# Performance work log

Measured on AMD Instinct MI355X. Metric: run time of the kernel, lower is better.

## Reference

```python
import jax, jax.numpy as jnp
import numpy as np

N, E, G = 20000, 640000, 64
D_IN, H, C, D_OUT = 256, 4, 64, 32
HC = H * C


def gat_layer(x, W, a_src, a_dst, b, src, dst, n_nodes, heads, ch):
    # x: [N, F_in], W: [F_in, H*C]
    h = (x @ W).reshape(n_nodes, heads, ch)          # [N,H,C]
    es = jnp.einsum('nhc,hc->nh', h, a_src)          # [N,H]
    ed = jnp.einsum('nhc,hc->nh', h, a_dst)
    e = jax.nn.leaky_relu(es[src] + ed[dst], 0.2)    # [Etot,H]
    m = jax.ops.segment_max(e, dst, num_segments=n_nodes)
    m = jnp.where(jnp.isfinite(m), m, 0.0)
    ex = jnp.exp(e - m[dst])
    denom = jax.ops.segment_sum(ex, dst, num_segments=n_nodes)
    alpha = ex / jnp.maximum(denom[dst], 1e-16)      # softmax over in-edges per dst
    out = jax.ops.segment_sum(alpha[:, :, None] * h[src], dst, num_segments=n_nodes)
    return out.reshape(n_nodes, heads * ch) + b


def setup_inputs() -> dict:
    key = jax.random.key(0)
    ks = jax.random.split(key, 14)
    g1 = 1.0 / np.sqrt(D_IN)
    g2 = 1.0 / np.sqrt(HC)
    inp = {
        'x': jax.random.normal(ks[0], (N, D_IN), jnp.float32),
        'edge_index': jax.random.randint(ks[1], (2, E), 0, N, jnp.int64 if jax.config.jax_enable_x64 else jnp.int32),
        'batch': jnp.sort(jax.random.randint(ks[2], (N,), 0, G)),
        'W1': jax.random.normal(ks[3], (D_IN, HC), jnp.float32) * g1,
        'a_src1': jax.random.normal(ks[4], (H, C), jnp.float32) * g2,
        'a_dst1': jax.random.normal(ks[5], (H, C), jnp.float32) * g2,
        'b1': jnp.zeros((HC,), jnp.float32),
        'W2': jax.random.normal(ks[6], (HC, HC), jnp.float32) * g2,
        'a_src2': jax.random.normal(ks[7], (H, C), jnp.float32) * g2,
        'a_dst2': jax.random.normal(ks[8], (H, C), jnp.float32) * g2,
        'b2': jnp.zeros((HC,), jnp.float32),
        'Wp': jax.random.normal(ks[9], (HC, D_OUT), jnp.float32) * g2,
        'bp': jnp.zeros((D_OUT,), jnp.float32),
    }
    return inp


def reference(x, edge_index, batch, W1, a_src1, a_dst1, b1, W2, a_src2, a_dst2, b2, Wp, bp):
    # add self-loops (PyG GATConv default)
    loop = jnp.arange(N, dtype=edge_index.dtype)
    src = jnp.concatenate([edge_index[0], loop])
    dst = jnp.concatenate([edge_index[1], loop])
    x1 = jax.nn.relu(gat_layer(x, W1, a_src1, a_dst1, b1, src, dst, N, H, C))
    # dropout p=0.6 is identity in eval mode
    x2 = jax.nn.relu(gat_layer(x1, W2, a_src2, a_dst2, b2, src, dst, N, H, C))
    node_scores = x2 @ Wp + bp                        # [N, D_OUT]
    sums = jax.ops.segment_sum(node_scores, batch, num_segments=G)
    counts = jax.ops.segment_sum(jnp.ones((N,), node_scores.dtype), batch, num_segments=G)
    return sums / jnp.maximum(counts, 1.0)[:, None]   # [G, D_OUT]
```

## Files before the change

### kernel.cpp

```cpp
#include <hip/hip_runtime.h>
#include <hip/hip_bf16.h>
#include <cstdint>

#define NNODES 20000
#define NEDGES 640000
#define ETOT   (NEDGES + NNODES)
#define NGROUP 64
#define HC     256
#define DOUT   32
#define EBLK   5120
#define NBLK   (NEDGES / EBLK)
#define CBLK   ((NNODES + 255) / 256)
#define GBLK   (NNODES / 16)
#define GPITCH 1280

typedef short bf16x8 __attribute__((ext_vector_type(8)));
typedef short s16x4  __attribute__((ext_vector_type(4)));
typedef float f32x4  __attribute__((ext_vector_type(4)));
typedef float f32x2  __attribute__((ext_vector_type(2)));
typedef int   s32x4  __attribute__((ext_vector_type(4)));
typedef unsigned int u32x4 __attribute__((ext_vector_type(4)));

__device__ __forceinline__ float b2f(__hip_bfloat16 v) { return __bfloat162float(v); }
__device__ __forceinline__ float bs2f(short v) {
    union { unsigned int u; float f; } c; c.u = ((unsigned int)(unsigned short)v) << 16; return c.f;
}
__device__ __forceinline__ short f2bs(float v) {
    __hip_bfloat16 b = __float2bfloat16(v);
    union { __hip_bfloat16 b; short s; } u; u.b = b; return u.s;
}
__device__ __forceinline__ float ldf(const void* __restrict__ p, size_t i, int bf) {
    return bf ? __bfloat162float(((const __hip_bfloat16*)p)[i]) : ((const float*)p)[i];
}
__device__ __forceinline__ int ld_idx(const int* __restrict__ p, size_t i, int f64) {
    return f64 ? p[2 * i] : p[i];
}
__device__ __forceinline__ int probe_edge64(const int* __restrict__ ei) {
    int l = threadIdx.x & 63;
    int zeros = 0;
#pragma unroll
    for (int r = 0; r < 4; r++)
        zeros += __popcll(__ballot(ei[2 * (r * 64 + l) + 1] == 0));
    return (zeros > 200) ? 1 : 0;
}
__device__ __forceinline__ int probe_xbf(const unsigned int* __restrict__ xw) {
    int l = threadIdx.x & 63;
    int ones = 0;
#pragma unroll
    for (int r = 0; r < 4; r++)
        ones += __popcll(__ballot((xw[r * 64 + l] >> 14) & 1));
    return (ones < 64) ? 1 : 0;
}

__global__ __launch_bounds__(256) void k_setup(const unsigned int* __restrict__ xw,
                                               const int* __restrict__ ei,
                                               const void* __restrict__ W1, const void* __restrict__ W2,
                                               __hip_bfloat16* __restrict__ Wt1,
                                               __hip_bfloat16* __restrict__ Wt2,
                                               int* __restrict__ H,
                                               float* __restrict__ sx, int* __restrict__ cnt,
                                               int* __restrict__ flag) {
    __shared__ int hl[NNODES];
    int t = threadIdx.x, b = blockIdx.x;
    if (b < NBLK) {
        int f = probe_edge64(ei);
        s32x4* hl4 = reinterpret_cast<s32x4*>(hl);
        for (int i = t; i < NNODES / 4; i += 256) hl4[i] = (s32x4){0, 0, 0, 0};
        __syncthreads();
        int s0 = b * EBLK;
        if (f) {
            const int* d64 = ei + 2 * NEDGES;
            for (int i0 = s0; i0 < s0 + EBLK; i0 += 512) {
                int i = i0 + 2 * t;
                s32x4 v = *reinterpret_cast<const s32x4*>(d64 + 2 * (size_t)i);
                atomicAdd(&hl[v[0]], 1);
                atomicAdd(&hl[v[2]], 1);
            }
        } else {
            const int* d32 = ei + NEDGES;
            for (int i0 = s0; i0 < s0 + EBLK; i0 += 1024) {
                int i = i0 + 4 * t;
                s32x4 v = *reinterpret_cast<const s32x4*>(d32 + i);
                atomicAdd(&hl[v[0]], 1); atomicAdd(&hl[v[1]], 1);
                atomicAdd(&hl[v[2]], 1); atomicAdd(&hl[v[3]], 1);
            }
        }
        __syncthreads();
        s32x4* Hb4 = reinterpret_cast<s32x4*>(H + (size_t)b * NNODES);
        for (int i = t; i < NNODES / 4; i += 256) Hb4[i] = hl4[i];
    } else {
        int bf = probe_xbf(xw);
        int i = (b - NBLK) * 256 + t;
        int which = i >> 16;
        int j = i & 65535;
        int k = j >> 8, n = j & 255;
        const void* W = which ? W2 : W1;
        __hip_bfloat16* Wt = which ? Wt2 : Wt1;
        Wt[(size_t)n * 256 + k] = __float2bfloat16(ldf(W, (size_t)k * 256 + n, bf));
        if (b == NBLK) {
            for (int q = t; q < NGROUP * HC; q += 256) sx[q] = 0.f;
            if (t < NGROUP) cnt[t] = 0;
            int f = probe_edge64(ei);
            if (t == 0) { flag[0] = f; flag[1] = bf; }
        }
    }
}

__global__ __launch_bounds__(256) void k_colsum(const int* __restrict__ H,
                                                int* __restrict__ deg,
                                                int* __restrict__ bsum) {
    __shared__ int wred[4];
    int t = threadIdx.x, n = blockIdx.x * 256 + t;
    int s = 0;
    if (n < NNODES) {
#pragma unroll 5
        for (int b = 0; b < NBLK; b++) s += H[(size_t)b * NNODES + n];
        s += 1;
        deg[n] = s;
    }
    int r = s;
#pragma unroll
    for (int o = 1; o < 64; o <<= 1) r += __shfl_xor(r, o);
    if ((t & 63) == 0) wred[t >> 6] = r;
    __syncthreads();
    if (t == 0) bsum[blockIdx.x] = wred[0] + wred[1] + wred[2] + wred[3];
}

__global__ __launch_bounds__(256) void k_base(int* __restrict__ H,
                                              const int* __restrict__ deg,
                                              const int* __restrict__ bsum,
                                              int* __restrict__ off,
                                              int* __restrict__ csr) {
    __shared__ int wtot[4];
    __shared__ int boff_s;
    int t = threadIdx.x, blk = blockIdx.x;
    int n = blk * 256 + t;
    int d = (n < NNODES) ? deg[n] : 0;
    int lane = t & 63, w = t >> 6;
    int sc = d;
#pragma unroll
    for (int o = 1; o < 64; o <<= 1) {
        int u = __shfl_up(sc, o);
        if (lane >= o) sc += u;
    }
    if (lane == 63) wtot[w] = sc;
    if (w == 0) {
        int v = (lane < blk) ? bsum[lane] : 0;
        if (lane + 64 < blk) v += bsum[lane + 64];
#pragma unroll
        for (int o = 1; o < 64; o <<= 1) v += __shfl_xor(v, o);
        if (lane == 0) boff_s = v;
    }
    __syncthreads();
    int woff = 0;
    for (int i = 0; i < w; i++) woff += wtot[i];
    int excl = woff + sc - d;
    if (blk == 0 && t == 0) off[NNODES] = ETOT;
    if (n < NNODES) {
        int o0 = boff_s + excl;
        off[n] = o0;
        csr[o0] = n;
        int run = o0 + 1;
#pragma unroll 5
        for (int b = 0; b < NBLK; b++) {
            size_t idx = (size_t)b * NNODES + n;
            int tt = H[idx];
            H[idx] = run;
            run += tt;
        }
    }
}

__global__ __launch_bounds__(256) void k_scatter2(const int* __restrict__ ei,
                                                  const int* __restrict__ H,
                                                  int* __restrict__ csr,
                                                  const int* __restrict__ flag) {
    __shared__ int base_l[NNODES];
    int t = threadIdx.x, b = blockIdx.x, f = flag[0];
    const s32x4* Hb4 = reinterpret_cast<const s32x4*>(H + (size_t)b * NNODES);
    s32x4* bl4 = reinterpret_cast<s32x4*>(base_l);
    for (int i = t; i < NNODES / 4; i += 256) bl4[i] = Hb4[i];
    __syncthreads();
    int s0 = b * EBLK;
    if (f) {
        const int* d64 = ei + 2 * NEDGES;
        for (int i0 = s0; i0 < s0 + EBLK; i0 += 512) {
            int i = i0 + 2 * t;
            s32x4 sv = *reinterpret_cast<const s32x4*>(ei + 2 * (size_t)i);
            s32x4 dv = *reinterpret_cast<const s32x4*>(d64 + 2 * (size_t)i);
            int p0 = atomicAdd(&base_l[dv[0]], 1);
            csr[p0] = sv[0];
            int p1 = atomicAdd(&base_l[dv[2]], 1);
            csr[p1] = sv[2];
        }
    } else {
        const int* d32 = ei + NEDGES;
        for (int i0 = s0; i0 < s0 + EBLK; i0 += 1024) {
            int i = i0 + 4 * t;
            s32x4 sv = *reinterpret_cast<const s32x4*>(ei + i);
            s32x4 dv = *reinterpret_cast<const s32x4*>(d32 + i);
#pragma unroll
            for (int k = 0; k < 4; k++) {
                int p = atomicAdd(&base_l[dv[k]], 1);
                csr[p] = sv[k];
            }
        }
    }
}

__global__ __launch_bounds__(256) void k_gemm(const void* __restrict__ A,
                                              const __hip_bfloat16* __restrict__ Bt,
                                              __hip_bfloat16* __restrict__ Hout,
                                              const void* __restrict__ a_src,
                                              const void* __restrict__ a_dst,
                                              float* __restrict__ es4, float* __restrict__ ed4,
                                              float* __restrict__ gpart,
                                              const int* __restrict__ flag, int force_bf) {
    __shared__ u32x4 hst4[512];
    int bf   = flag[1];
    int abf  = force_bf | bf;
    int w    = threadIdx.x >> 6;
    int lane = threadIdx.x & 63;
    int mr   = lane & 15;
    int quad = lane >> 4;
    int r0   = blockIdx.x * 16;
    f32x4 acc[4];
#pragma unroll
    for (int j = 0; j < 4; j++) acc[j] = (f32x4){0.f, 0.f, 0.f, 0.f};
    size_t rowoff = (size_t)(r0 + mr) * HC;
    const __hip_bfloat16* Btw = Bt + (size_t)w * 64 * HC;
    for (int kk = 0; kk < HC; kk += 32) {
        bf16x8 a;
        if (abf) {
            a = *reinterpret_cast<const bf16x8*>((const __hip_bfloat16*)A + rowoff + kk + quad * 8);
        } else {
            const float* af = (const float*)A + rowoff + kk + quad * 8;
            f32x4 lo = *reinterpret_cast<const f32x4*>(af);
            f32x4 hi = *reinterpret_cast<const f32x4*>(af + 4);
#pragma unroll
            for (int ii = 0; ii < 4; ii++) { a[ii] = f2bs(lo[ii]); a[ii + 4] = f2bs(hi[ii]); }
        }
#pragma unroll
        for (int j = 0; j < 4; j++) {
            bf16x8 b = *reinterpret_cast<const bf16x8*>(Btw + (size_t)(j * 16 + mr) * HC + kk + quad * 8);
            acc[j] = __builtin_amdgcn_mfma_f32_16x16x32_bf16(a, b, acc[j], 0, 0, 0);
        }
    }
    short* hst = reinterpret_cast<short*>(hst4);
#pragma unroll
    for (int j = 0; j < 4; j++)
#pragma unroll
        for (int r = 0; r < 4; r++)
            hst[(quad * 4 + r) * HC + w * 64 + j * 16 + mr] = f2bs(acc[j][r]);
    float ps[4] = {0.f, 0.f, 0.f, 0.f}, pd[4] = {0.f, 0.f, 0.f, 0.f};
#pragma unroll
    for (int j = 0; j < 4; j++) {
        float asv = ldf(a_src, (size_t)(w * 64 + j * 16 + mr), bf);
        float adv = ldf(a_dst, (size_t)(w * 64 + j * 16 + mr), bf);
#pragma unroll
        for (int r = 0; r < 4; r++) {
            ps[r] = fmaf(acc[j][r], asv, ps[r]);
            pd[r] = fmaf(acc[j][r], adv, pd[r]);
        }
    }
#pragma unroll
    for (int o = 1; o < 16; o <<= 1)
#pragma unroll
        for (int r = 0; r < 4; r++) {
            ps[r] += __shfl_xor(ps[r], o);
            pd[r] += __shfl_xor(pd[r], o);
        }
    float pm = fmaxf(fmaxf(ps[0], ps[1]), fmaxf(ps[2], ps[3]));
    pm = fmaxf(pm, __shfl_xor(pm, 16));
    pm = fmaxf(pm, __shfl_xor(pm, 32));
    if (lane == 0) gpart[w * GPITCH + blockIdx.x] = pm;
    if (mr == 0)
#pragma unroll
        for (int r = 0; r < 4; r++) {
            int row = r0 + quad * 4 + r;
            es4[(size_t)row * 4 + w] = ps[r];
            ed4[(size_t)row * 4 + w] = pd[r];
        }
    __syncthreads();
    u32x4* dst = reinterpret_cast<u32x4*>((short*)Hout + (size_t)r0 * HC);
    dst[threadIdx.x]       = hst4[threadIdx.x];
    dst[threadIdx.x + 256] = hst4[threadIdx.x + 256];
}

__global__ __launch_bounds__(256) void k_agg(const __hip_bfloat16* __restrict__ Hb,
                                             const float* __restrict__ es4, const float* __restrict__ ed4,
                                             const void* __restrict__ bias,
                                             const int* __restrict__ off, const int* __restrict__ csr,
                                             const float* __restrict__ gpart,
                                             const int* __restrict__ flag,
                                             __hip_bfloat16* __restrict__ out) {
    __shared__ float p_lds[4][4][64];
    __shared__ int   s_lds[4][64];
    __shared__ float gm_lds[4];
    int wv = threadIdx.x >> 6;
    int l  = threadIdx.x & 63;
    int half = l >> 5;
    int hl   = l & 31;
    int hd8  = hl >> 3;
    int bf = flag[1];
    {
        float m = -INFINITY;
        for (int i = l; i < GBLK; i += 64) m = fmaxf(m, gpart[wv * GPITCH + i]);
#pragma unroll
        for (int o = 32; o; o >>= 1) m = fmaxf(m, __shfl_xor(m, o));
        if (l == 0) gm_lds[wv] = m;
    }
    __syncthreads();
    f32x4 gm = (f32x4){gm_lds[0], gm_lds[1], gm_lds[2], gm_lds[3]};
    int n0 = blockIdx.x * 4 + wv;
    for (int n = n0; n < NNODES; n += 10000) {
        int base = off[n], deg = off[n + 1] - base;
        f32x4 edv = *reinterpret_cast<const f32x4*>(ed4 + (size_t)n * 4);
        f32x4 M;
#pragma unroll
        for (int h = 0; h < 4; h++) {
            float t0 = gm[h] + edv[h];
            M[h] = (t0 > 0.f) ? t0 : 0.2f * t0;
        }
        f32x4 dsum = (f32x4){0.f, 0.f, 0.f, 0.f};
        f32x2 acc2[4];
#pragma unroll
        for (int d = 0; d < 4; d++) acc2[d] = (f32x2){0.f, 0.f};
        for (int c0 = 0; c0 < deg; c0 += 64) {
            int cn = min(deg - c0, 64);
            int s = 0;
            f32x4 pv = (f32x4){0.f, 0.f, 0.f, 0.f};
            if (l < cn) {
                s = csr[base + c0 + l];
                f32x4 e = *reinterpret_cast<const f32x4*>(es4 + (size_t)s * 4);
#pragma unroll
                for (int h = 0; h < 4; h++) {
                    float t = e[h] + edv[h];
                    t = (t > 0.f) ? t : 0.2f * t;
                    pv[h] = __expf(t - M[h]);
                }
            }
            s_lds[wv][l] = s;
#pragma unroll
            for (int h = 0; h < 4; h++) p_lds[wv][h][l] = pv[h];
#pragma unroll
            for (int h = 0; h < 4; h++) dsum[h] += pv[h];
            int jn = (cn + 15) & ~15;
            for (int j = 0; j < jn; j += 16) {
                int e0 = j + 8 * half;
                s32x4 sA = *reinterpret_cast<const s32x4*>(&s_lds[wv][e0]);
                s32x4 sB = *reinterpret_cast<const s32x4*>(&s_lds[wv][e0 + 4]);
                f32x4 pA = *reinterpret_cast<const f32x4*>(&p_lds[wv][hd8][e0]);
                f32x4 pB = *reinterpret_cast<const f32x4*>(&p_lds[wv][hd8][e0 + 4]);
                u32x4 hv[8];
#pragma unroll
                for (int i = 0; i < 8; i++) {
                    int sj = (i < 4) ? sA[i & 3] : sB[i & 3];
                    hv[i] = *reinterpret_cast<const u32x4*>(Hb + (size_t)sj * HC + hl * 8);
                }
#pragma unroll
                for (int i = 0; i < 8; i++) {
                    float p = (i < 4) ? pA[i & 3] : pB[i & 3];
#pragma unroll
                    for (int d = 0; d < 4; d++) {
                        unsigned int u = hv[i][d];
                        f32x2 h2;
                        h2.x = __uint_as_float(u << 16);
                        h2.y = __uint_as_float(u & 0xFFFF0000u);
                        acc2[d] += h2 * p;
                    }
                }
            }
        }
#pragma unroll
        for (int o = 32; o; o >>= 1)
#pragma unroll
            for (int h = 0; h < 4; h++) dsum[h] += __shfl_xor(dsum[h], o);
#pragma unroll
        for (int d = 0; d < 4; d++) {
            acc2[d].x += __shfl_xor(acc2[d].x, 32);
            acc2[d].y += __shfl_xor(acc2[d].y, 32);
        }
        float rinv = 1.0f / fmaxf(dsum[hd8], 1e-16f);
        if (half == 0) {
            bf16x8 ov;
#pragma unroll
            for (int d = 0; d < 4; d++) {
                float v0 = acc2[d].x * rinv + ldf(bias, (size_t)hl * 8 + 2 * d, bf);
                float v1 = acc2[d].y * rinv + ldf(bias, (size_t)hl * 8 + 2 * d + 1, bf);
                ov[2 * d]     = f2bs(fmaxf(v0, 0.f));
                ov[2 * d + 1] = f2bs(fmaxf(v1, 0.f));
            }
            *reinterpret_cast<bf16x8*>(out + (size_t)n * HC + hl * 8) = ov;
        }
    }
}

__global__ __launch_bounds__(256) void k_groupsum(const __hip_bfloat16* __restrict__ X2,
                                                  const int* __restrict__ batch,
                                                  float* __restrict__ sx, int* __restrict__ cnt,
                                                  const int* __restrict__ flag) {
    const int RPB = NNODES / 250;
    int b = blockIdx.x, f = flag[0];
    int sub = threadIdx.x >> 6, l = threadIdx.x & 63;
    int r = b * RPB + sub;
    f32x4 acc = (f32x4){0.f, 0.f, 0.f, 0.f};
    int curg = ld_idx(batch, r, f);
    int cacc = 0;
    for (int k = 0; k < RPB / 4; k++, r += 4) {
        int g = ld_idx(batch, r, f);
        if (g != curg) {
#pragma unroll
            for (int c = 0; c < 4; c++) atomicAdd(&sx[(size_t)curg * HC + l * 4 + c], acc[c]);
            if (l == 0) atomicAdd(&cnt[curg], cacc);
            acc = (f32x4){0.f, 0.f, 0.f, 0.f}; cacc = 0; curg = g;
        }
        s16x4 hv = *reinterpret_cast<const s16x4*>(X2 + (size_t)r * HC + l * 4);
#pragma unroll
        for (int c = 0; c < 4; c++) acc[c] += bs2f(hv[c]);
        cacc++;
    }
#pragma unroll
    for (int c = 0; c < 4; c++) atomicAdd(&sx[(size_t)curg * HC + l * 4 + c], acc[c]);
    if (l == 0) atomicAdd(&cnt[curg], cacc);
}

__global__ __launch_bounds__(256) void k_final(const float* __restrict__ sx,
                                               const void* __restrict__ Wp,
                                               const void* __restrict__ bp,
                                               const int* __restrict__ cnt,
                                               const int* __restrict__ flag,
                                               void* __restrict__ out) {
    __shared__ float red[8][32];
    int g = blockIdx.x, t = threadIdx.x;
    int c = t & 31, seg = t >> 5;
    int bf = flag[1];
    const float* sxg = sx + (size_t)g * HC;
    float a = 0.f;
#pragma unroll
    for (int k = 0; k < 32; k++) {
        int kk = seg * 32 + k;
        a = fmaf(sxg[kk], ldf(Wp, (size_t)kk * DOUT + c, bf), a);
    }
    red[seg][c] = a;
    __syncthreads();
    if (t < 32) {
        float s = 0.f;
#pragma unroll
        for (int i = 0; i < 8; i++) s += red[i][t];
        int ct = cnt[g];
        float v = (ct > 0) ? (s / ct + ldf(bp, (size_t)t, bf)) : 0.f;
        if (bf) ((__hip_bfloat16*)out)[g * DOUT + t] = __float2bfloat16(v);
        else    ((float*)out)[g * DOUT + t]          = v;
    }
}

extern "C" void kernel_launch(void* const* d_in, const int* in_sizes, int n_in,
                              void* d_out, int out_size, void* d_ws, size_t ws_size,
                              hipStream_t stream) {
    (void)in_sizes; (void)n_in; (void)out_size; (void)ws_size;
    const void* x   = d_in[0];
    const int*  ei  = (const int*)d_in[1];
    const int*  bat = (const int*)d_in[2];
    const void* W1  = d_in[3];
    const void* as1 = d_in[4];
    const void* ad1 = d_in[5];
    const void* b1  = d_in[6];
    const void* W2  = d_in[7];
    const void* as2 = d_in[8];
    const void* ad2 = d_in[9];
    const void* b2  = d_in[10];
    const void* Wp  = d_in[11];
    const void* bp  = d_in[12];

    char* ws = (char*)d_ws;
    size_t o = 0;
    auto alloc = [&](size_t bytes) -> char* {
        char* p = ws + o;
        o += (bytes + 255) & ~(size_t)255;
        return p;
    };
    __hip_bfloat16* hb  = (__hip_bfloat16*)alloc((size_t)NNODES * HC * 2);
    __hip_bfloat16* xb  = (__hip_bfloat16*)alloc((size_t)NNODES * HC * 2);
    __hip_bfloat16* xb2 = (__hip_bfloat16*)alloc((size_t)NNODES * HC * 2);
    __hip_bfloat16* Wt1 = (__hip_bfloat16*)alloc((size_t)HC * HC * 2);
    __hip_bfloat16* Wt2 = (__hip_bfloat16*)alloc((size_t)HC * HC * 2);
    float* es = (float*)alloc((size_t)NNODES * 4 * 4);
    float* ed = (float*)alloc((size_t)NNODES * 4 * 4);
    int* H    = (int*)alloc((size_t)NBLK * NNODES * 4);
    int* deg  = (int*)alloc((size_t)NNODES * 4);
    int* off  = (int*)alloc((size_t)(NNODES + 1) * 4);
    int* csr  = (int*)alloc((size_t)ETOT * 4);
    int* bsum = (int*)alloc((size_t)CBLK * 4);
    float* gpart = (float*)alloc((size_t)4 * GPITCH * 4);
    float* sx = (float*)alloc((size_t)NGROUP * HC * 4);
    int* cnt  = (int*)alloc(256);
    int* flag = (int*)alloc(256);

    k_setup<<<NBLK + 512, 256, 0, stream>>>((const unsigned int*)x, ei, W1, W2,
                                            Wt1, Wt2, H, sx, cnt, flag);
    k_colsum<<<CBLK, 256, 0, stream>>>(H, deg, bsum);
    k_base<<<CBLK, 256, 0, stream>>>(H, deg, bsum, off, csr);
    k_scatter2<<<NBLK, 256, 0, stream>>>(ei, H, csr, flag);

    k_gemm<<<GBLK, 256, 0, stream>>>(x, Wt1, hb, as1, ad1, es, ed, gpart, flag, 0);
    k_agg<<<2500, 256, 0, stream>>>(hb, es, ed, b1, off, csr, gpart, flag, xb);

    k_gemm<<<GBLK, 256, 0, stream>>>(xb, Wt2, hb, as2, ad2, es, ed, gpart, flag, 1);
    k_agg<<<2500, 256, 0, stream>>>(hb, es, ed, b2, off, csr, gpart, flag, xb2);

    k_groupsum<<<250, 256, 0, stream>>>(xb2, bat, sx, cnt, flag);
    k_final<<<NGROUP, 256, 0, stream>>>(sx, Wp, bp, cnt, flag, d_out);
}
```

Baseline: 307.9 us.

## Fuse whole GAT pipeline into one cooperative persistent kernel with grid syncs

Replaces the ten separate kernel launches with a single cooperative kernel of 768 persistent blocks that runs every stage and separates them with grid.sync(). The edge histogram and scatter now work on half the node range per pass, which cuts LDS use to 40KB so several blocks fit per CU and the grid stays co-resident. The first GEMM runs alongside the CSR scatter on otherwise idle blocks. Format probes are recomputed per block instead of being passed through a flag buffer, and the old multi-kernel path is kept as a fallback if the cooperative launch fails. The two-pass histogram doubles edge reads, and the grid barriers plus the reduced block count for agg and gemm may cost parallelism.

```diff
diff --git a/kernel.cpp b/kernel.cpp
--- a/kernel.cpp
+++ b/kernel.cpp
@@ -1,6 +1,9 @@
 #include <hip/hip_runtime.h>
+#include <hip/hip_cooperative_groups.h>
 #include <hip/hip_bf16.h>
 #include <cstdint>
+
+namespace cg = cooperative_groups;
 
 #define NNODES 20000
 #define NEDGES 640000
@@ -13,6 +16,9 @@
 #define CBLK   ((NNODES + 255) / 256)
 #define GBLK   (NNODES / 16)
 #define GPITCH 1280
+#define MB     768
+#define HALFN  10240
+#define SMEMB  (HALFN * 4)
 
 typedef short bf16x8 __attribute__((ext_vector_type(8)));
 typedef short s16x4  __attribute__((ext_vector_type(4)));
@@ -21,7 +27,6 @@
 typedef int   s32x4  __attribute__((ext_vector_type(4)));
 typedef unsigned int u32x4 __attribute__((ext_vector_type(4)));
 
-__device__ __forceinline__ float b2f(__hip_bfloat16 v) { return __bfloat162float(v); }
 __device__ __forceinline__ float bs2f(short v) {
     union { unsigned int u; float f; } c; c.u = ((unsigned int)(unsigned short)v) << 16; return c.f;
 }
@@ -52,20 +57,15 @@
     return (ones < 64) ? 1 : 0;
 }
 
-__global__ __launch_bounds__(256) void k_setup(const unsigned int* __restrict__ xw,
-                                               const int* __restrict__ ei,
-                                               const void* __restrict__ W1, const void* __restrict__ W2,
-                                               __hip_bfloat16* __restrict__ Wt1,
-                                               __hip_bfloat16* __restrict__ Wt2,
-                                               int* __restrict__ H,
-                                               float* __restrict__ sx, int* __restrict__ cnt,
-                                               int* __restrict__ flag) {
-    __shared__ int hl[NNODES];
-    int t = threadIdx.x, b = blockIdx.x;
-    if (b < NBLK) {
-        int f = probe_edge64(ei);
-        s32x4* hl4 = reinterpret_cast<s32x4*>(hl);
-        for (int i = t; i < NNODES / 4; i += 256) hl4[i] = (s32x4){0, 0, 0, 0};
+
+__device__ __forceinline__ void dev_hist(int b, int f, const int* __restrict__ ei,
+                                         int* __restrict__ H, int* hl) {
+    int t = threadIdx.x;
+    for (int pass = 0; pass < 2; ++pass) {
+        int nbase = pass * HALFN;
+        int span = NNODES - nbase; if (span > HALFN) span = HALFN;
+        s32x4* h4 = reinterpret_cast<s32x4*>(hl);
+        for (int i = t; i < HALFN / 4; i += 256) h4[i] = (s32x4){0, 0, 0, 0};
         __syncthreads();
         int s0 = b * EBLK;
         if (f) {
@@ -73,44 +73,45 @@
             for (int i0 = s0; i0 < s0 + EBLK; i0 += 512) {
                 int i = i0 + 2 * t;
                 s32x4 v = *reinterpret_cast<const s32x4*>(d64 + 2 * (size_t)i);
-                atomicAdd(&hl[v[0]], 1);
-                atomicAdd(&hl[v[2]], 1);
+                unsigned d0 = (unsigned)(v[0] - nbase), d1 = (unsigned)(v[2] - nbase);
+                if (d0 < (unsigned)span) atomicAdd(&hl[d0], 1);
+                if (d1 < (unsigned)span) atomicAdd(&hl[d1], 1);
             }
         } else {
             const int* d32 = ei + NEDGES;
             for (int i0 = s0; i0 < s0 + EBLK; i0 += 1024) {
                 int i = i0 + 4 * t;
                 s32x4 v = *reinterpret_cast<const s32x4*>(d32 + i);
-                atomicAdd(&hl[v[0]], 1); atomicAdd(&hl[v[1]], 1);
-                atomicAdd(&hl[v[2]], 1); atomicAdd(&hl[v[3]], 1);
+#pragma unroll
+                for (int k = 0; k < 4; k++) {
+                    unsigned d = (unsigned)(v[k] - nbase);
+                    if (d < (unsigned)span) atomicAdd(&hl[d], 1);
+                }
             }
         }
         __syncthreads();
-        s32x4* Hb4 = reinterpret_cast<s32x4*>(H + (size_t)b * NNODES);
-        for (int i = t; i < NNODES / 4; i += 256) Hb4[i] = hl4[i];
-    } else {
-        int bf = probe_xbf(xw);
-        int i = (b - NBLK) * 256 + t;
-        int which = i >> 16;
-        int j = i & 65535;
-        int k = j >> 8, n = j & 255;
-        const void* W = which ? W2 : W1;
-        __hip_bfloat16* Wt = which ? Wt2 : Wt1;
-        Wt[(size_t)n * 256 + k] = __float2bfloat16(ldf(W, (size_t)k * 256 + n, bf));
-        if (b == NBLK) {
-            for (int q = t; q < NGROUP * HC; q += 256) sx[q] = 0.f;
-            if (t < NGROUP) cnt[t] = 0;
-            int f = probe_edge64(ei);
-            if (t == 0) { flag[0] = f; flag[1] = bf; }
-        }
-    }
-}
-
-__global__ __launch_bounds__(256) void k_colsum(const int* __restrict__ H,
-                                                int* __restrict__ deg,
-                                                int* __restrict__ bsum) {
-    __shared__ int wred[4];
-    int t = threadIdx.x, n = blockIdx.x * 256 + t;
+        int* Hb = H + (size_t)b * NNODES + nbase;
+        for (int i = t; i < span; i += 256) Hb[i] = hl[i];
+        if (pass == 0) __syncthreads();
+    }
+}
+
+__device__ __forceinline__ void dev_wt(int u, int bf,
+                                       const void* __restrict__ W1, const void* __restrict__ W2,
+                                       __hip_bfloat16* __restrict__ Wt1, __hip_bfloat16* __restrict__ Wt2) {
+    int i = u * 256 + threadIdx.x;
+    int which = i >> 16;
+    int j = i & 65535;
+    int k = j >> 8, n = j & 255;
+    const void* W = which ? W2 : W1;
+    __hip_bfloat16* Wt = which ? Wt2 : Wt1;
+    Wt[(size_t)n * 256 + k] = __float2bfloat16(ldf(W, (size_t)k * 256 + n, bf));
+}
+
+__device__ __forceinline__ void dev_colsum(int blk, const int* __restrict__ H,
+                                           int* __restrict__ deg, int* __restrict__ bsum,
+                                           int* wred) {
+    int t = threadIdx.x, n = blk * 256 + t;
     int s = 0;
     if (n < NNODES) {
 #pragma unroll 5
@@ -123,17 +124,14 @@
     for (int o = 1; o < 64; o <<= 1) r += __shfl_xor(r, o);
     if ((t & 63) == 0) wred[t >> 6] = r;
     __syncthreads();
-    if (t == 0) bsum[blockIdx.x] = wred[0] + wred[1] + wred[2] + wred[3];
-}
-
-__global__ __launch_bounds__(256) void k_base(int* __restrict__ H,
-                                              const int* __restrict__ deg,
-                                              const int* __restrict__ bsum,
-                                              int* __restrict__ off,
-                                              int* __restrict__ csr) {
-    __shared__ int wtot[4];
-    __shared__ int boff_s;
-    int t = threadIdx.x, blk = blockIdx.x;
+    if (t == 0) bsum[blk] = wred[0] + wred[1] + wred[2] + wred[3];
+}
+
+__device__ __forceinline__ void dev_base(int blk, int* __restrict__ H,
+                                         const int* __restrict__ deg, const int* __restrict__ bsum,
+                                         int* __restrict__ off, int* __restrict__ csr,
+                                         int* scr ) {
+    int t = threadIdx.x;
     int n = blk * 256 + t;
     int d = (n < NNODES) ? deg[n] : 0;
     int lane = t & 63, w = t >> 6;
@@ -143,21 +141,21 @@
         int u = __shfl_up(sc, o);
         if (lane >= o) sc += u;
     }
-    if (lane == 63) wtot[w] = sc;
+    if (lane == 63) scr[w] = sc;
     if (w == 0) {
         int v = (lane < blk) ? bsum[lane] : 0;
         if (lane + 64 < blk) v += bsum[lane + 64];
 #pragma unroll
         for (int o = 1; o < 64; o <<= 1) v += __shfl_xor(v, o);
-        if (lane == 0) boff_s = v;
+        if (lane == 0) scr[4] = v;
     }
     __syncthreads();
     int woff = 0;
-    for (int i = 0; i < w; i++) woff += wtot[i];
+    for (int i = 0; i < w; i++) woff += scr[i];
     int excl = woff + sc - d;
     if (blk == 0 && t == 0) off[NNODES] = ETOT;
     if (n < NNODES) {
-        int o0 = boff_s + excl;
+        int o0 = scr[4] + excl;
         off[n] = o0;
         csr[o0] = n;
         int run = o0 + 1;
@@ -171,59 +169,56 @@
     }
 }
 
-__global__ __launch_bounds__(256) void k_scatter2(const int* __restrict__ ei,
-                                                  const int* __restrict__ H,
-                                                  int* __restrict__ csr,
-                                                  const int* __restrict__ flag) {
-    __shared__ int base_l[NNODES];
-    int t = threadIdx.x, b = blockIdx.x, f = flag[0];
-    const s32x4* Hb4 = reinterpret_cast<const s32x4*>(H + (size_t)b * NNODES);
-    s32x4* bl4 = reinterpret_cast<s32x4*>(base_l);
-    for (int i = t; i < NNODES / 4; i += 256) bl4[i] = Hb4[i];
-    __syncthreads();
-    int s0 = b * EBLK;
-    if (f) {
-        const int* d64 = ei + 2 * NEDGES;
-        for (int i0 = s0; i0 < s0 + EBLK; i0 += 512) {
-            int i = i0 + 2 * t;
-            s32x4 sv = *reinterpret_cast<const s32x4*>(ei + 2 * (size_t)i);
-            s32x4 dv = *reinterpret_cast<const s32x4*>(d64 + 2 * (size_t)i);
-            int p0 = atomicAdd(&base_l[dv[0]], 1);
-            csr[p0] = sv[0];
-            int p1 = atomicAdd(&base_l[dv[2]], 1);
-            csr[p1] = sv[2];
-        }
-    } else {
-        const int* d32 = ei + NEDGES;
-        for (int i0 = s0; i0 < s0 + EBLK; i0 += 1024) {
-            int i = i0 + 4 * t;
-            s32x4 sv = *reinterpret_cast<const s32x4*>(ei + i);
-            s32x4 dv = *reinterpret_cast<const s32x4*>(d32 + i);
-#pragma unroll
-            for (int k = 0; k < 4; k++) {
-                int p = atomicAdd(&base_l[dv[k]], 1);
-                csr[p] = sv[k];
+__device__ __forceinline__ void dev_scatter(int b, int f, const int* __restrict__ ei,
+                                            const int* __restrict__ H, int* __restrict__ csr,
+                                            int* hl) {
+    int t = threadIdx.x;
+    for (int pass = 0; pass < 2; ++pass) {
+        int nbase = pass * HALFN;
+        int span = NNODES - nbase; if (span > HALFN) span = HALFN;
+        const int* Hb = H + (size_t)b * NNODES + nbase;
+        for (int i = t; i < span; i += 256) hl[i] = Hb[i];
+        __syncthreads();
+        int s0 = b * EBLK;
+        if (f) {
+            const int* d64 = ei + 2 * NEDGES;
+            for (int i0 = s0; i0 < s0 + EBLK; i0 += 512) {
+                int i = i0 + 2 * t;
+                s32x4 sv = *reinterpret_cast<const s32x4*>(ei + 2 * (size_t)i);
+                s32x4 dv = *reinterpret_cast<const s32x4*>(d64 + 2 * (size_t)i);
+                unsigned d0 = (unsigned)(dv[0] - nbase), d1 = (unsigned)(dv[2] - nbase);
+                if (d0 < (unsigned)span) { int p = atomicAdd(&hl[d0], 1); csr[p] = sv[0]; }
+                if (d1 < (unsigned)span) { int p = atomicAdd(&hl[d1], 1); csr[p] = sv[2]; }
             }
-        }
-    }
-}
-
-__global__ __launch_bounds__(256) void k_gemm(const void* __restrict__ A,
-                                              const __hip_bfloat16* __restrict__ Bt,
-                                              __hip_bfloat16* __restrict__ Hout,
-                                              const void* __restrict__ a_src,
-                                              const void* __restrict__ a_dst,
-                                              float* __restrict__ es4, float* __restrict__ ed4,
-                                              float* __restrict__ gpart,
-                                              const int* __restrict__ flag, int force_bf) {
-    __shared__ u32x4 hst4[512];
-    int bf   = flag[1];
-    int abf  = force_bf | bf;
+        } else {
+            const int* d32 = ei + NEDGES;
+            for (int i0 = s0; i0 < s0 + EBLK; i0 += 1024) {
+                int i = i0 + 4 * t;
+                s32x4 sv = *reinterpret_cast<const s32x4*>(ei + i);
+                s32x4 dv = *reinterpret_cast<const s32x4*>(d32 + i);
+#pragma unroll
+                for (int k = 0; k < 4; k++) {
+                    unsigned d = (unsigned)(dv[k] - nbase);
+                    if (d < (unsigned)span) { int p = atomicAdd(&hl[d], 1); csr[p] = sv[k]; }
+                }
+            }
+        }
+        if (pass == 0) __syncthreads();
+    }
+}
+
+__device__ __forceinline__ void dev_gemm(int tile, const void* __restrict__ A,
+                                         const __hip_bfloat16* __restrict__ Bt,
+                                         __hip_bfloat16* __restrict__ Hout,
+                                         const void* __restrict__ a_src, const void* __restrict__ a_dst,
+                                         float* __restrict__ es4, float* __restrict__ ed4,
+                                         float* __restrict__ gpart, int bf, int abf,
+                                         u32x4* hst4) {
     int w    = threadIdx.x >> 6;
     int lane = threadIdx.x & 63;
     int mr   = lane & 15;
     int quad = lane >> 4;
-    int r0   = blockIdx.x * 16;
+    int r0   = tile * 16;
     f32x4 acc[4];
 #pragma unroll
     for (int j = 0; j < 4; j++) acc[j] = (f32x4){0.f, 0.f, 0.f, 0.f};
@@ -273,7 +268,7 @@
     float pm = fmaxf(fmaxf(ps[0], ps[1]), fmaxf(ps[2], ps[3]));
     pm = fmaxf(pm, __shfl_xor(pm, 16));
     pm = fmaxf(pm, __shfl_xor(pm, 32));
-    if (lane == 0) gpart[w * GPITCH + blockIdx.x] = pm;
+    if (lane == 0) gpart[w * GPITCH + tile] = pm;
     if (mr == 0)
 #pragma unroll
         for (int r = 0; r < 4; r++) {
@@ -285,35 +280,39 @@
     u32x4* dst = reinterpret_cast<u32x4*>((short*)Hout + (size_t)r0 * HC);
     dst[threadIdx.x]       = hst4[threadIdx.x];
     dst[threadIdx.x + 256] = hst4[threadIdx.x + 256];
-}
-
-__global__ __launch_bounds__(256) void k_agg(const __hip_bfloat16* __restrict__ Hb,
-                                             const float* __restrict__ es4, const float* __restrict__ ed4,
-                                             const void* __restrict__ bias,
-                                             const int* __restrict__ off, const int* __restrict__ csr,
-                                             const float* __restrict__ gpart,
-                                             const int* __restrict__ flag,
-                                             __hip_bfloat16* __restrict__ out) {
-    __shared__ float p_lds[4][4][64];
-    __shared__ int   s_lds[4][64];
-    __shared__ float gm_lds[4];
+    __syncthreads();
+}
+
+__device__ __forceinline__ void dev_agg(int n0, int nstr,
+                                        const __hip_bfloat16* __restrict__ Hb,
+                                        const float* __restrict__ es4, const float* __restrict__ ed4,
+                                        const void* __restrict__ bias,
+                                        const int* __restrict__ off, const int* __restrict__ csr,
+                                        const float* __restrict__ gpart, int bf,
+                                        __hip_bfloat16* __restrict__ out, int* smem) {
+    float (*p_lds)[64] = reinterpret_cast<float(*)[64]>(smem);
     int wv = threadIdx.x >> 6;
     int l  = threadIdx.x & 63;
     int half = l >> 5;
     int hl   = l & 31;
     int hd8  = hl >> 3;
-    int bf = flag[1];
+    float* pw = (float*)(smem) + wv * 256;
+    int*   sw = smem + 1024 + wv * 64;
+    float* gm_s = (float*)(smem + 1280);
     {
-        float m = -INFINITY;
-        for (int i = l; i < GBLK; i += 64) m = fmaxf(m, gpart[wv * GPITCH + i]);
+        const float* gp = gpart + wv * GPITCH;
+        float ma = -INFINITY, mb = -INFINITY;
+        int i = l;
+        for (; i + 64 < GBLK; i += 128) { ma = fmaxf(ma, gp[i]); mb = fmaxf(mb, gp[i + 64]); }
+        if (i < GBLK) ma = fmaxf(ma, gp[i]);
+        float m = fmaxf(ma, mb);
 #pragma unroll
         for (int o = 32; o; o >>= 1) m = fmaxf(m, __shfl_xor(m, o));
-        if (l == 0) gm_lds[wv] = m;
+        if (l == 0) gm_s[wv] = m;
     }
     __syncthreads();
-    f32x4 gm = (f32x4){gm_lds[0], gm_lds[1], gm_lds[2], gm_lds[3]};
-    int n0 = blockIdx.x * 4 + wv;
-    for (int n = n0; n < NNODES; n += 10000) {
+    f32x4 gm = (f32x4){gm_s[0], gm_s[1], gm_s[2], gm_s[3]};
+    for (int n = n0; n < NNODES; n += nstr) {
         int base = off[n], deg = off[n + 1] - base;
         f32x4 edv = *reinterpret_cast<const f32x4*>(ed4 + (size_t)n * 4);
         f32x4 M;
@@ -340,18 +339,18 @@
                     pv[h] = __expf(t - M[h]);
                 }
             }
-            s_lds[wv][l] = s;
-#pragma unroll
-            for (int h = 0; h < 4; h++) p_lds[wv][h][l] = pv[h];
+            sw[l] = s;
+#pragma unroll
+            for (int h = 0; h < 4; h++) pw[h * 64 + l] = pv[h];
 #pragma unroll
             for (int h = 0; h < 4; h++) dsum[h] += pv[h];
             int jn = (cn + 15) & ~15;
             for (int j = 0; j < jn; j += 16) {
                 int e0 = j + 8 * half;
-                s32x4 sA = *reinterpret_cast<const s32x4*>(&s_lds[wv][e0]);
-                s32x4 sB = *reinterpret_cast<const s32x4*>(&s_lds[wv][e0 + 4]);
-                f32x4 pA = *reinterpret_cast<const f32x4*>(&p_lds[wv][hd8][e0]);
-                f32x4 pB = *reinterpret_cast<const f32x4*>(&p_lds[wv][hd8][e0 + 4]);
+                s32x4 sA = *reinterpret_cast<const s32x4*>(&sw[e0]);
+                s32x4 sB = *reinterpret_cast<const s32x4*>(&sw[e0 + 4]);
+                f32x4 pA = *reinterpret_cast<const f32x4*>(&pw[hd8 * 64 + e0]);
+                f32x4 pB = *reinterpret_cast<const f32x4*>(&pw[hd8 * 64 + e0 + 4]);
                 u32x4 hv[8];
 #pragma unroll
                 for (int i = 0; i < 8; i++) {
@@ -394,14 +393,13 @@
             *reinterpret_cast<bf16x8*>(out + (size_t)n * HC + hl * 8) = ov;
         }
     }
-}
-
-__global__ __launch_bounds__(256) void k_groupsum(const __hip_bfloat16* __restrict__ X2,
-                                                  const int* __restrict__ batch,
-                                                  float* __restrict__ sx, int* __restrict__ cnt,
-                                                  const int* __restrict__ flag) {
+    (void)p_lds;
+}
+
+__device__ __forceinline__ void dev_groupsum(int b, int f, const __hip_bfloat16* __restrict__ X2,
+                                             const int* __restrict__ batch,
+                                             float* __restrict__ sx, int* __restrict__ cnt) {
     const int RPB = NNODES / 250;
-    int b = blockIdx.x, f = flag[0];
     int sub = threadIdx.x >> 6, l = threadIdx.x & 63;
     int r = b * RPB + sub;
     f32x4 acc = (f32x4){0.f, 0.f, 0.f, 0.f};
@@ -425,16 +423,12 @@
     if (l == 0) atomicAdd(&cnt[curg], cacc);
 }
 
-__global__ __launch_bounds__(256) void k_final(const float* __restrict__ sx,
-                                               const void* __restrict__ Wp,
-                                               const void* __restrict__ bp,
-                                               const int* __restrict__ cnt,
-                                               const int* __restrict__ flag,
-                                               void* __restrict__ out) {
-    __shared__ float red[8][32];
-    int g = blockIdx.x, t = threadIdx.x;
+__device__ __forceinline__ void dev_final(int g, int bf, const float* __restrict__ sx,
+                                          const void* __restrict__ Wp, const void* __restrict__ bp,
+                                          const int* __restrict__ cnt, void* __restrict__ out,
+                                          float* red ) {
+    int t = threadIdx.x;
     int c = t & 31, seg = t >> 5;
-    int bf = flag[1];
     const float* sxg = sx + (size_t)g * HC;
     float a = 0.f;
 #pragma unroll
@@ -442,17 +436,127 @@
         int kk = seg * 32 + k;
         a = fmaf(sxg[kk], ldf(Wp, (size_t)kk * DOUT + c, bf), a);
     }
-    red[seg][c] = a;
+    red[seg * 32 + c] = a;
     __syncthreads();
     if (t < 32) {
         float s = 0.f;
 #pragma unroll
-        for (int i = 0; i < 8; i++) s += red[i][t];
+        for (int i = 0; i < 8; i++) s += red[i * 32 + t];
         int ct = cnt[g];
         float v = (ct > 0) ? (s / ct + ldf(bp, (size_t)t, bf)) : 0.f;
         if (bf) ((__hip_bfloat16*)out)[g * DOUT + t] = __float2bfloat16(v);
         else    ((float*)out)[g * DOUT + t]          = v;
     }
+}
+
+__global__ void k_mega(const void* x, const int* ei, const int* bat,
+                       const void* W1, const void* as1, const void* ad1, const void* b1,
+                       const void* W2, const void* as2, const void* ad2, const void* b2,
+                       const void* Wp, const void* bp,
+                       __hip_bfloat16* hb, __hip_bfloat16* xb, __hip_bfloat16* xb2,
+                       __hip_bfloat16* Wt1, __hip_bfloat16* Wt2,
+                       float* es, float* ed, int* H, int* deg, int* off, int* csr,
+                       int* bsum, float* gpart, float* sx, int* cnt, void* out) {
+    extern __shared__ int smem[];
+    cg::grid_group grid = cg::this_grid();
+    int bid = blockIdx.x, t = threadIdx.x;
+    int f  = probe_edge64(ei);
+    int bf = probe_xbf((const unsigned int*)x);
+
+    if (bid < NBLK) {
+        dev_hist(bid, f, ei, H, smem);
+    } else {
+        for (int u = bid - NBLK; u < 512; u += MB - NBLK)
+            dev_wt(u, bf, W1, W2, Wt1, Wt2);
+        if (bid == NBLK) {
+            for (int q = t; q < NGROUP * HC; q += 256) sx[q] = 0.f;
+            if (t < NGROUP) cnt[t] = 0;
+        }
+    }
+    grid.sync();
+    if (bid < CBLK) dev_colsum(bid, H, deg, bsum, smem);
+    grid.sync();
+    if (bid < CBLK) dev_base(bid, H, deg, bsum, off, csr, smem);
+    grid.sync();
+    if (bid < NBLK) {
+        dev_scatter(bid, f, ei, H, csr, smem);
+    } else {
+        for (int tile = bid - NBLK; tile < GBLK; tile += MB - NBLK)
+            dev_gemm(tile, x, Wt1, hb, as1, ad1, es, ed, gpart, bf, bf, (u32x4*)smem);
+    }
+    grid.sync();
+    dev_agg(bid * 4 + (t >> 6), MB * 4, hb, es, ed, b1, off, csr, gpart, bf, xb, smem);
+    grid.sync();
+    for (int tile = bid; tile < GBLK; tile += MB)
+        dev_gemm(tile, xb, Wt2, hb, as2, ad2, es, ed, gpart, bf, 1, (u32x4*)smem);
+    grid.sync();
+    dev_agg(bid * 4 + (t >> 6), MB * 4, hb, es, ed, b2, off, csr, gpart, bf, xb2, smem);
+    grid.sync();
+    if (bid < 250) dev_groupsum(bid, f, xb2, bat, sx, cnt);
+    grid.sync();
+    if (bid < NGROUP) dev_final(bid, bf, sx, Wp, bp, cnt, out, (float*)smem);
+}
+
+__global__ __launch_bounds__(256) void fk_setup(const void* x, const int* ei,
+                                                const void* W1, const void* W2,
+                                                __hip_bfloat16* Wt1, __hip_bfloat16* Wt2,
+                                                int* H, float* sx, int* cnt) {
+    __shared__ int smem[HALFN];
+    int bid = blockIdx.x, t = threadIdx.x;
+    if (bid < NBLK) {
+        int f = probe_edge64(ei);
+        dev_hist(bid, f, ei, H, smem);
+    } else {
+        int bf = probe_xbf((const unsigned int*)x);
+        dev_wt(bid - NBLK, bf, W1, W2, Wt1, Wt2);
+        if (bid == NBLK) {
+            for (int q = t; q < NGROUP * HC; q += 256) sx[q] = 0.f;
+            if (t < NGROUP) cnt[t] = 0;
+        }
+    }
+}
+__global__ __launch_bounds__(256) void fk_colsum(const int* H, int* deg, int* bsum) {
+    __shared__ int wred[4];
+    dev_colsum(blockIdx.x, H, deg, bsum, wred);
+}
+__global__ __launch_bounds__(256) void fk_base(int* H, const int* deg, const int* bsum,
+                                               int* off, int* csr) {
+    __shared__ int scr[5];
+    dev_base(blockIdx.x, H, deg, bsum, off, csr, scr);
+}
+__global__ __launch_bounds__(256) void fk_scatter(const int* ei, const int* H, int* csr) {
+    __shared__ int smem[HALFN];
+    int f = probe_edge64(ei);
+    dev_scatter(blockIdx.x, f, ei, H, csr, smem);
+}
+__global__ __launch_bounds__(256) void fk_gemm(const void* x, const void* A,
+                                               const __hip_bfloat16* Bt, __hip_bfloat16* Hout,
+                                               const void* a_src, const void* a_dst,
+                                               float* es4, float* ed4, float* gpart, int force_bf) {
+    __shared__ u32x4 hst4[512];
+    int bf = probe_xbf((const unsigned int*)x);
+    dev_gemm(blockIdx.x, A, Bt, Hout, a_src, a_dst, es4, ed4, gpart, bf, force_bf | bf, hst4);
+}
+__global__ __launch_bounds__(256) void fk_agg(const void* x, const __hip_bfloat16* Hb,
+                                              const float* es4, const float* ed4,
+                                              const void* bias, const int* off, const int* csr,
+                                              const float* gpart, __hip_bfloat16* out) {
+    __shared__ int smem[1284];
+    int bf = probe_xbf((const unsigned int*)x);
+    dev_agg(blockIdx.x * 4 + (threadIdx.x >> 6), MB * 4, Hb, es4, ed4, bias, off, csr,
+            gpart, bf, out, smem);
+}
+__global__ __launch_bounds__(256) void fk_groupsum(const int* ei, const __hip_bfloat16* X2,
+                                                   const int* batch, float* sx, int* cnt) {
+    int f = probe_edge64(ei);
+    dev_groupsum(blockIdx.x, f, X2, batch, sx, cnt);
+}
+__global__ __launch_bounds__(256) void fk_final(const void* x, const float* sx,
+                                                const void* Wp, const void* bp,
+                                                const int* cnt, void* out) {
+    __shared__ float red[256];
+    int bf = probe_xbf((const unsigned int*)x);
+    dev_final(blockIdx.x, bf, sx, Wp, bp, cnt, out, red);
 }
 
 extern "C" void kernel_launch(void* const* d_in, const int* in_sizes, int n_in,
@@ -495,20 +599,31 @@
     float* gpart = (float*)alloc((size_t)4 * GPITCH * 4);
     float* sx = (float*)alloc((size_t)NGROUP * HC * 4);
     int* cnt  = (int*)alloc(256);
-    int* flag = (int*)alloc(256);
-
-    k_setup<<<NBLK + 512, 256, 0, stream>>>((const unsigned int*)x, ei, W1, W2,
-                                            Wt1, Wt2, H, sx, cnt, flag);
-    k_colsum<<<CBLK, 256, 0, stream>>>(H, deg, bsum);
-    k_base<<<CBLK, 256, 0, stream>>>(H, deg, bsum, off, csr);
-    k_scatter2<<<NBLK, 256, 0, stream>>>(ei, H, csr, flag);
-
-    k_gemm<<<GBLK, 256, 0, stream>>>(x, Wt1, hb, as1, ad1, es, ed, gpart, flag, 0);
-    k_agg<<<2500, 256, 0, stream>>>(hb, es, ed, b1, off, csr, gpart, flag, xb);
-
-    k_gemm<<<GBLK, 256, 0, stream>>>(xb, Wt2, hb, as2, ad2, es, ed, gpart, flag, 1);
-    k_agg<<<2500, 256, 0, stream>>>(hb, es, ed, b2, off, csr, gpart, flag, xb2);
-
-    k_groupsum<<<250, 256, 0, stream>>>(xb2, bat, sx, cnt, flag);
-    k_final<<<NGROUP, 256, 0, stream>>>(sx, Wp, bp, cnt, flag, d_out);
-}
+    void* outp = d_out;
+
+    void* kargs[] = {
+        (void*)&x, (void*)&ei, (void*)&bat,
+        (void*)&W1, (void*)&as1, (void*)&ad1, (void*)&b1,
+        (void*)&W2, (void*)&as2, (void*)&ad2, (void*)&b2,
+        (void*)&Wp, (void*)&bp,
+        (void*)&hb, (void*)&xb, (void*)&xb2, (void*)&Wt1, (void*)&Wt2,
+        (void*)&es, (void*)&ed, (void*)&H, (void*)&deg, (void*)&off, (void*)&csr,
+        (void*)&bsum, (void*)&gpart, (void*)&sx, (void*)&cnt, (void*)&outp
+    };
+    hipError_t err = hipLaunchCooperativeKernel(reinterpret_cast<void*>(k_mega),
+                                                dim3(MB), dim3(256), kargs,
+                                                (unsigned)SMEMB, stream);
+    if (err != hipSuccess) {
+        (void)hipGetLastError();
+        fk_setup<<<NBLK + 512, 256, 0, stream>>>(x, ei, W1, W2, Wt1, Wt2, H, sx, cnt);
+        fk_colsum<<<CBLK, 256, 0, stream>>>(H, deg, bsum);
+        fk_base<<<CBLK, 256, 0, stream>>>(H, deg, bsum, off, csr);
+        fk_scatter<<<NBLK, 256, 0, stream>>>(ei, H, csr);
+        fk_gemm<<<GBLK, 256, 0, stream>>>(x, x, Wt1, hb, as1, ad1, es, ed, gpart, 0);
+        fk_agg<<<MB, 256, 0, stream>>>(x, hb, es, ed, b1, off, csr, gpart, xb);
+        fk_gemm<<<GBLK, 256, 0, stream>>>(x, xb, Wt2, hb, as2, ad2, es, ed, gpart, 1);
+        fk_agg<<<MB, 256, 0, stream>>>(x, hb, es, ed, b2, off, csr, gpart, xb2);
+        fk_groupsum<<<250, 256, 0, stream>>>(ei, xb2, bat, sx, cnt);
+        fk_final<<<NGROUP, 256, 0, stream>>>(x, sx, Wp, bp, cnt, d_out);
+    }
+}
```

Result: slower. 1.016 ms (+230.0%).
